# Kernel tuning notes

Hardware: AMD Instinct MI355X
Metric: run time of the kernel (lower is better)

## Reference

```python
import jax, jax.numpy as jnp
import numpy as np

EPS = 0.1  # FAConv default eps


def setup_inputs() -> dict:
    key = jax.random.key(0)
    k1, k2, k3, k4, k5 = jax.random.split(key, 5)
    N, D, E, Dout = 50000, 128, 600000, 128
    x = jax.random.normal(k1, (N, D), dtype=jnp.float32)
    edge_index = jax.random.randint(k2, (2, E), 0, N, dtype=jnp.int64)
    # glorot-style scale for att vectors (Linear(D,1)) and weight matrix
    att_l = jax.random.normal(k3, (D,), dtype=jnp.float32) * (1.0 / np.sqrt(D))
    att_r = jax.random.normal(k4, (D,), dtype=jnp.float32) * (1.0 / np.sqrt(D))
    weight = jax.random.normal(k5, (D, Dout), dtype=jnp.float32) * np.sqrt(6.0 / (D + Dout))
    bias = jnp.zeros((Dout,), dtype=jnp.float32)
    return {"x": x, "edge_index": edge_index, "att_l": att_l, "att_r": att_r,
            "weight": weight, "bias": bias}


def reference(x, edge_index, att_l, att_r, weight, bias):
    N, D = x.shape
    # gcn_norm with add_self_loops=True
    loops = jnp.arange(N, dtype=edge_index.dtype)
    row = jnp.concatenate([edge_index[0], loops])  # source nodes
    col = jnp.concatenate([edge_index[1], loops])  # target nodes
    deg = jax.ops.segment_sum(jnp.ones_like(col, dtype=x.dtype), col, num_segments=N)
    dinv = jnp.where(deg > 0, jax.lax.rsqrt(jnp.maximum(deg, 1e-12)), 0.0)
    norm = dinv[row] * dinv[col]  # [E+N]
    # FAConv attention: alpha = tanh(att_l . x_j + att_r . x_i)
    al = x @ att_l  # [N]
    ar = x @ att_r  # [N]
    a = jnp.tanh(al[row] + ar[col])  # per-edge
    msg = x[row] * (a * norm)[:, None]  # [E+N, D]
    agg = jax.ops.segment_sum(msg, col, num_segments=N)
    h = agg + EPS * x  # x_0 == x in SAGNN.forward
    return h @ weight + bias
```

## Files before the change

kernel.cpp:

```cpp
#include <hip/hip_runtime.h>
#include <hip/hip_bf16.h>

#define FA_EPS 0.1f
#define BUCKET_M 48

typedef _Float16 half8  __attribute__((ext_vector_type(8)));
typedef _Float16 half4v __attribute__((ext_vector_type(4)));
typedef float    f32x4  __attribute__((ext_vector_type(4)));


__global__ __launch_bounds__(256) void k_node_prep(
    const float* __restrict__ x,
    const float* __restrict__ att_l,
    const float* __restrict__ att_r,
    float4* __restrict__ P, unsigned int* __restrict__ cursor,
    _Float16* __restrict__ x16, int N)
{
    int wave = (int)((blockIdx.x * blockDim.x + threadIdx.x) >> 6);
    int lane = threadIdx.x & 63;
    int half = lane >> 5;
    int sl   = lane & 31;
    int node = wave * 2 + half;
    if (node >= N) return;
    const float4* xr = (const float4*)(x + (size_t)node * 128);
    float4 v  = xr[sl];
    float4 l4 = ((const float4*)att_l)[sl];
    float4 r4 = ((const float4*)att_r)[sl];
    half4v hv;
    hv[0] = (_Float16)v.x; hv[1] = (_Float16)v.y;
    hv[2] = (_Float16)v.z; hv[3] = (_Float16)v.w;
    *((half4v*)(x16 + (size_t)node * 128) + sl) = hv;
    float pal = v.x * l4.x + v.y * l4.y + v.z * l4.z + v.w * l4.w;
    float par = v.x * r4.x + v.y * r4.y + v.z * r4.z + v.w * r4.w;
    #pragma unroll
    for (int off = 16; off > 0; off >>= 1) {
        pal += __shfl_xor(pal, off);
        par += __shfl_xor(par, off);
    }
    if (sl == 0) {
        float4 pv;
        pv.x = pal; pv.y = par;
        pv.z = __uint_as_float(0u); pv.w = 0.f;
        P[node] = pv;
        cursor[node] = 0u;
    }
}

__global__ __launch_bounds__(256) void k_degree_wconv(
    const int* __restrict__ ei, float4* __restrict__ P,
    const float* __restrict__ w, _Float16* __restrict__ wt, int E)
{
    int g = (int)(blockIdx.x * blockDim.x + threadIdx.x);
    if (g < 128 * 128) {
        int k = g >> 7, n = g & 127;
        wt[n * 128 + k] = (_Float16)w[k * 128 + n];
    }
    if (g < E) {
        int t = ei[E + g];
        atomicAdd((unsigned int*)P + 4 * (size_t)t + 2, 1u);
    }
}

__global__ __launch_bounds__(256) void k_fill(
    const int* __restrict__ ei,
    const float4* __restrict__ P,
    unsigned int* __restrict__ cursor,
    int2* __restrict__ csr, int E)
{
    int e = (int)(blockIdx.x * blockDim.x + threadIdx.x);
    if (e >= E) return;
    int s = ei[e];
    int t = ei[E + e];
    float4 ps = P[s];
    float4 pt = P[t];
    float dinv_s = rsqrtf((float)(__float_as_uint(ps.z) + 1u));
    float dinv_t = rsqrtf((float)(__float_as_uint(pt.z) + 1u));
    float alpha = tanhf(ps.x + pt.y) * dinv_s * dinv_t;
    unsigned int pos = atomicAdd(&cursor[t], 1u);
    if (pos < BUCKET_M)
        csr[(size_t)t * BUCKET_M + pos] = make_int2(s, __float_as_int(alpha));
}

__global__ __launch_bounds__(256) void k_gather(
    const _Float16* __restrict__ x16,
    const int2* __restrict__ csr,
    const float4* __restrict__ P,
    _Float16* __restrict__ h16, int N)
{
    int wave = (int)((blockIdx.x * blockDim.x + threadIdx.x) >> 6);
    int lane = threadIdx.x & 63;
    int g  = lane >> 4;
    int sl = lane & 15;
    int t  = wave * 4 + g;
    bool valid = t < N;
    int tc = valid ? t : N - 1;
    float4 p = P[tc];
    unsigned int deg = __float_as_uint(p.z);
    unsigned int cnt = deg < BUCKET_M ? deg : BUCKET_M;
    if (!valid) cnt = 0u;
    const int2* cs = csr + (size_t)tc * BUCKET_M;
    float acc[8];
    #pragma unroll
    for (int c = 0; c < 8; ++c) acc[c] = 0.f;
    for (unsigned int j = 0; j < cnt; j += 4) {
        int2 e[4];
        #pragma unroll
        for (int u = 0; u < 4; ++u) {
            unsigned int idx = j + u;
            if (idx >= cnt) idx = cnt - 1;
            e[u] = cs[idx];
        }
        #pragma unroll
        for (int u = 0; u < 4; ++u)
            if (j + u >= cnt) e[u].y = 0;
        half8 v[4];
        #pragma unroll
        for (int u = 0; u < 4; ++u)
            v[u] = *((const half8*)(x16 + (size_t)e[u].x * 128) + sl);
        #pragma unroll
        for (int u = 0; u < 4; ++u) {
            float a = __int_as_float(e[u].y);
            #pragma unroll
            for (int c = 0; c < 8; ++c) acc[c] += a * (float)v[u][c];
        }
    }
    float dinv_t = rsqrtf((float)(deg + 1u));
    float coef = tanhf(p.x + p.y) * dinv_t * dinv_t + FA_EPS;
    half8 vt = *((const half8*)(x16 + (size_t)tc * 128) + sl);
    #pragma unroll
    for (int c = 0; c < 8; ++c) acc[c] += coef * (float)vt[c];
    if (valid) {
        half8 hv;
        #pragma unroll
        for (int c = 0; c < 8; ++c) hv[c] = (_Float16)acc[c];
        *((half8*)(h16 + (size_t)t * 128) + sl) = hv;
    }
}

__global__ __launch_bounds__(256) void k_matmul_mfma(
    const _Float16* __restrict__ h16,
    const _Float16* __restrict__ wt,
    const float* __restrict__ bias,
    float* __restrict__ out, int N)
{
    __shared__ _Float16 wl[128 * 136];
    int tid = threadIdx.x;
    {
        const float* wsrc = (const float*)wt;
        float* wdst = (float*)wl;
        #pragma unroll
        for (int i = tid; i < 8192; i += 256)
            wdst[(i >> 6) * 68 + (i & 63)] = wsrc[i];
    }
    __syncthreads();
    int wv   = tid >> 6;
    int lane = tid & 63;
    int m    = lane & 15;
    int quad = lane >> 4;
    int r0 = (int)blockIdx.x * 64 + wv * 16;
    f32x4 acc[8];
    #pragma unroll
    for (int t = 0; t < 8; ++t) acc[t] = (f32x4)0.f;
    const _Float16* arow = h16 + (size_t)(r0 + m) * 128 + quad * 8;
    #pragma unroll
    for (int k0 = 0; k0 < 128; k0 += 32) {
        half8 a = *(const half8*)(arow + k0);
        #pragma unroll
        for (int t = 0; t < 8; ++t) {
            const _Float16* bp = wl + (size_t)(t * 16 + m) * 136 + quad * 8 + k0;
            half8 b = *(const half8*)bp;
            acc[t] = __builtin_amdgcn_mfma_f32_16x16x32_f16(a, b, acc[t], 0, 0, 0);
        }
    }
    int orow = r0 + quad * 4;
    #pragma unroll
    for (int t = 0; t < 8; ++t) {
        int col = t * 16 + m;
        float bc = bias[col];
        #pragma unroll
        for (int rg = 0; rg < 4; ++rg) {
            int r = orow + rg;
            if (r < N) out[(size_t)r * 128 + col] = acc[t][rg] + bc;
        }
    }
}

extern "C" void kernel_launch(void* const* d_in, const int* in_sizes, int n_in,
                              void* d_out, int out_size, void* d_ws, size_t ws_size,
                              hipStream_t stream)
{
    const float* x     = (const float*)d_in[0];
    const int*   ei    = (const int*)d_in[1];
    const float* att_l = (const float*)d_in[2];
    const float* att_r = (const float*)d_in[3];
    const float* w     = (const float*)d_in[4];
    const float* bias  = (const float*)d_in[5];
    float* out = (float*)d_out;

    const int N  = in_sizes[0] / 128;
    const int E  = in_sizes[1] / 2;
    const int NP = ((N + 63) / 64) * 64;

    char* ws = (char*)d_ws;
    _Float16*     h16    = (_Float16*)ws;
    _Float16*     x16    = h16 + (size_t)NP * 128;
    float4*       P      = (float4*)(x16 + (size_t)N * 128);
    unsigned int* cursor = (unsigned int*)(P + N);
    int2*         csr    = (int2*)(cursor + N);
    _Float16*     wt     = (_Float16*)(csr + (size_t)N * BUCKET_M);

    {
        int waves = (N + 1) / 2;
        k_node_prep<<<(waves * 64 + 255) / 256, 256, 0, stream>>>(
            x, att_l, att_r, P, cursor, x16, N);
    }
    k_degree_wconv<<<(E + 255) / 256, 256, 0, stream>>>(ei, P, w, wt, E);
    k_fill<<<(E + 255) / 256, 256, 0, stream>>>(ei, P, cursor, csr, E);
    {
        int waves = (N + 3) / 4;
        k_gather<<<(waves * 64 + 255) / 256, 256, 0, stream>>>(
            x16, csr, P, h16, N);
    }
    k_matmul_mfma<<<NP / 64, 256, 0, stream>>>(h16, wt, bias, out, N);
}
```

Measured before the change: 180.1 us.

## Merge degree count into CSR fill and defer normalization to gather

The separate degree-counting pass is removed. The bucket-fill atomic cursor now doubles as the in-degree counter, and edges store only the tanh attention value. Normalization by source and target inverse sqrt degree moves into the gather kernel, which reads each neighbor's degree alongside its feature row. The weight transpose is folded into the node prep kernel and a memset zeroes the degree array. This saves one pass over the edge list and one kernel launch, at the cost of an extra random 4-byte load per edge inside the gather loop.

```diff
diff --git a/kernel.cpp b/kernel.cpp
--- a/kernel.cpp
+++ b/kernel.cpp
@@ -7,16 +7,21 @@
 typedef _Float16 half8  __attribute__((ext_vector_type(8)));
 typedef _Float16 half4v __attribute__((ext_vector_type(4)));
 typedef float    f32x4  __attribute__((ext_vector_type(4)));
-
 
 __global__ __launch_bounds__(256) void k_node_prep(
     const float* __restrict__ x,
     const float* __restrict__ att_l,
     const float* __restrict__ att_r,
-    float4* __restrict__ P, unsigned int* __restrict__ cursor,
-    _Float16* __restrict__ x16, int N)
-{
-    int wave = (int)((blockIdx.x * blockDim.x + threadIdx.x) >> 6);
+    const float* __restrict__ w,
+    float* __restrict__ al, float* __restrict__ ar,
+    _Float16* __restrict__ x16, _Float16* __restrict__ wt, int N)
+{
+    int gtid = (int)(blockIdx.x * blockDim.x + threadIdx.x);
+    if (gtid < 128 * 128) {
+        int k = gtid >> 7, n = gtid & 127;
+        wt[n * 128 + k] = (_Float16)w[k * 128 + n];
+    }
+    int wave = gtid >> 6;
     int lane = threadIdx.x & 63;
     int half = lane >> 5;
     int sl   = lane & 31;
@@ -38,53 +43,32 @@
         par += __shfl_xor(par, off);
     }
     if (sl == 0) {
-        float4 pv;
-        pv.x = pal; pv.y = par;
-        pv.z = __uint_as_float(0u); pv.w = 0.f;
-        P[node] = pv;
-        cursor[node] = 0u;
-    }
-}
-
-__global__ __launch_bounds__(256) void k_degree_wconv(
-    const int* __restrict__ ei, float4* __restrict__ P,
-    const float* __restrict__ w, _Float16* __restrict__ wt, int E)
-{
-    int g = (int)(blockIdx.x * blockDim.x + threadIdx.x);
-    if (g < 128 * 128) {
-        int k = g >> 7, n = g & 127;
-        wt[n * 128 + k] = (_Float16)w[k * 128 + n];
-    }
-    if (g < E) {
-        int t = ei[E + g];
-        atomicAdd((unsigned int*)P + 4 * (size_t)t + 2, 1u);
-    }
-}
-
-__global__ __launch_bounds__(256) void k_fill(
+        al[node] = pal;
+        ar[node] = par;
+    }
+}
+
+__global__ __launch_bounds__(256) void k_edge(
     const int* __restrict__ ei,
-    const float4* __restrict__ P,
-    unsigned int* __restrict__ cursor,
+    const float* __restrict__ al, const float* __restrict__ ar,
+    unsigned int* __restrict__ deg,
     int2* __restrict__ csr, int E)
 {
     int e = (int)(blockIdx.x * blockDim.x + threadIdx.x);
     if (e >= E) return;
     int s = ei[e];
     int t = ei[E + e];
-    float4 ps = P[s];
-    float4 pt = P[t];
-    float dinv_s = rsqrtf((float)(__float_as_uint(ps.z) + 1u));
-    float dinv_t = rsqrtf((float)(__float_as_uint(pt.z) + 1u));
-    float alpha = tanhf(ps.x + pt.y) * dinv_s * dinv_t;
-    unsigned int pos = atomicAdd(&cursor[t], 1u);
+    float th = tanhf(al[s] + ar[t]);
+    unsigned int pos = atomicAdd(&deg[t], 1u);
     if (pos < BUCKET_M)
-        csr[(size_t)t * BUCKET_M + pos] = make_int2(s, __float_as_int(alpha));
+        csr[(size_t)t * BUCKET_M + pos] = make_int2(s, __float_as_int(th));
 }
 
 __global__ __launch_bounds__(256) void k_gather(
     const _Float16* __restrict__ x16,
     const int2* __restrict__ csr,
-    const float4* __restrict__ P,
+    const unsigned int* __restrict__ deg,
+    const float* __restrict__ al, const float* __restrict__ ar,
     _Float16* __restrict__ h16, int N)
 {
     int wave = (int)((blockIdx.x * blockDim.x + threadIdx.x) >> 6);
@@ -94,10 +78,10 @@
     int t  = wave * 4 + g;
     bool valid = t < N;
     int tc = valid ? t : N - 1;
-    float4 p = P[tc];
-    unsigned int deg = __float_as_uint(p.z);
-    unsigned int cnt = deg < BUCKET_M ? deg : BUCKET_M;
+    unsigned int dt = deg[tc];
+    unsigned int cnt = dt < BUCKET_M ? dt : BUCKET_M;
     if (!valid) cnt = 0u;
+    float dinv_t = rsqrtf((float)(dt + 1u));
     const int2* cs = csr + (size_t)tc * BUCKET_M;
     float acc[8];
     #pragma unroll
@@ -113,19 +97,22 @@
         #pragma unroll
         for (int u = 0; u < 4; ++u)
             if (j + u >= cnt) e[u].y = 0;
+        unsigned int ds[4];
         half8 v[4];
         #pragma unroll
-        for (int u = 0; u < 4; ++u)
-            v[u] = *((const half8*)(x16 + (size_t)e[u].x * 128) + sl);
-        #pragma unroll
         for (int u = 0; u < 4; ++u) {
-            float a = __int_as_float(e[u].y);
+            ds[u] = deg[e[u].x];
+            v[u]  = *((const half8*)(x16 + (size_t)e[u].x * 128) + sl);
+        }
+        #pragma unroll
+        for (int u = 0; u < 4; ++u) {
+            float a = __int_as_float(e[u].y)
+                    * rsqrtf((float)(ds[u] + 1u)) * dinv_t;
             #pragma unroll
             for (int c = 0; c < 8; ++c) acc[c] += a * (float)v[u][c];
         }
     }
-    float dinv_t = rsqrtf((float)(deg + 1u));
-    float coef = tanhf(p.x + p.y) * dinv_t * dinv_t + FA_EPS;
+    float coef = tanhf(al[tc] + ar[tc]) * dinv_t * dinv_t + FA_EPS;
     half8 vt = *((const half8*)(x16 + (size_t)tc * 128) + sl);
     #pragma unroll
     for (int c = 0; c < 8; ++c) acc[c] += coef * (float)vt[c];
@@ -202,24 +189,26 @@
     const int NP = ((N + 63) / 64) * 64;
 
     char* ws = (char*)d_ws;
-    _Float16*     h16    = (_Float16*)ws;
-    _Float16*     x16    = h16 + (size_t)NP * 128;
-    float4*       P      = (float4*)(x16 + (size_t)N * 128);
-    unsigned int* cursor = (unsigned int*)(P + N);
-    int2*         csr    = (int2*)(cursor + N);
-    _Float16*     wt     = (_Float16*)(csr + (size_t)N * BUCKET_M);
+    _Float16*     h16 = (_Float16*)ws;
+    _Float16*     x16 = h16 + (size_t)NP * 128;
+    float*        al  = (float*)(x16 + (size_t)N * 128);
+    float*        ar  = al + N;
+    unsigned int* deg = (unsigned int*)(ar + N);
+    int2*         csr = (int2*)(deg + N);
+    _Float16*     wt  = (_Float16*)(csr + (size_t)N * BUCKET_M);
+
+    hipMemsetAsync(deg, 0, (size_t)N * sizeof(unsigned int), stream);
 
     {
         int waves = (N + 1) / 2;
         k_node_prep<<<(waves * 64 + 255) / 256, 256, 0, stream>>>(
-            x, att_l, att_r, P, cursor, x16, N);
-    }
-    k_degree_wconv<<<(E + 255) / 256, 256, 0, stream>>>(ei, P, w, wt, E);
-    k_fill<<<(E + 255) / 256, 256, 0, stream>>>(ei, P, cursor, csr, E);
+            x, att_l, att_r, w, al, ar, x16, wt, N);
+    }
+    k_edge<<<(E + 255) / 256, 256, 0, stream>>>(ei, al, ar, deg, csr, E);
     {
         int waves = (N + 3) / 4;
         k_gather<<<(waves * 64 + 255) / 256, 256, 0, stream>>>(
-            x16, csr, P, h16, N);
+            x16, csr, deg, al, ar, h16, N);
     }
     k_matmul_mfma<<<NP / 64, 256, 0, stream>>>(h16, wt, bias, out, N);
 }
```

Measured after the change: 162.4 us. 9.8% less time.
